# Kernel tuning notes

Measured on AMD Instinct MI355X. Metric: run time of the kernel, lower is better.

Reference implementation:

```python
import jax, jax.numpy as jnp
import numpy as np

T, D, I, E, G, LG, K = 2048, 1024, 512, 32, 8, 4, 6
SI = 2 * I  # shared expert inter dim = n_shared_experts * inter_dim
ROUTE_SCALE = 1.0


def setup_inputs() -> dict:
    key = jax.random.key(0)
    ks = jax.random.split(key, 16)
    s = 0.02
    f = jnp.float32
    return {
        "x": jax.random.normal(ks[0], (T, D), f),
        "router_w": jax.random.normal(ks[1], (E, D), f) * s,
        "router_b": jax.random.normal(ks[2], (E,), f) * s,
        "W1": jax.random.normal(ks[3], (E, D, I), f) * s,
        "b1": jax.random.normal(ks[4], (E, I), f) * s,
        "W2": jax.random.normal(ks[5], (E, D, I), f) * s,
        "b2": jax.random.normal(ks[6], (E, I), f) * s,
        "W3": jax.random.normal(ks[7], (E, I, D), f) * s,
        "b3": jax.random.normal(ks[8], (E, D), f) * s,
        "sw1": jax.random.normal(ks[9], (D, SI), f) * s,
        "sb1": jax.random.normal(ks[10], (SI,), f) * s,
        "sw2": jax.random.normal(ks[11], (D, SI), f) * s,
        "sb2": jax.random.normal(ks[12], (SI,), f) * s,
        "sw3": jax.random.normal(ks[13], (SI, D), f) * s,
        "sb3": jax.random.normal(ks[14], (D,), f) * s,
    }


def _route(x, router_w, router_b):
    # Router: softmax scores (fp32), group-limited top-k.
    logits = x @ router_w.T + router_b                      # [T, E]
    scores = jax.nn.softmax(logits.astype(jnp.float32), axis=-1)
    original = scores
    sg = scores.reshape(x.shape[0], G, E // G)              # [T, G, E/G]
    # no router bias -> group score = sum of top-2 expert scores per group
    group_scores = jnp.sum(jax.lax.top_k(sg, 2)[0], axis=-1)  # [T, G]
    _, gidx = jax.lax.top_k(group_scores, LG)               # [T, LG]
    keep = jnp.zeros((x.shape[0], G), bool).at[jnp.arange(x.shape[0])[:, None], gidx].set(True)
    masked = jnp.where(keep[:, :, None], sg, -jnp.inf).reshape(x.shape[0], E)
    _, idx = jax.lax.top_k(masked, K)                       # [T, K]
    vals = jnp.take_along_axis(original, idx, axis=1) * ROUTE_SCALE
    return vals.astype(x.dtype), idx


def reference(x, router_w, router_b, W1, b1, W2, b2, W3, b3, sw1, sb1, sw2, sb2, sw3, sb3):
    vals, idx = _route(x, router_w, router_b)
    # dense gate matrix [T, E]; top-k indices per row are distinct
    gates = jnp.zeros((x.shape[0], E), x.dtype).at[jnp.arange(x.shape[0])[:, None], idx].set(vals)
    # routed experts: Expert(x) = W3 @ silu(w1(x) * w2(x))
    h1 = jnp.einsum('td,edi->tei', x, W1) + b1              # [T, E, I]
    h2 = jnp.einsum('td,edi->tei', x, W2) + b2
    h = jax.nn.silu(h1 * h2)
    y = jnp.einsum('tei,eid->td', h * gates[:, :, None], W3) + gates @ b3
    # shared expert
    z = jax.nn.silu((x @ sw1 + sb1) * (x @ sw2 + sb2)) @ sw3 + sb3
    return y + z
```

## Files before the change

### kernel.cpp

```cpp
#include <hip/hip_runtime.h>
#include <hip/hip_bf16.h>
#include <math.h>

#define T_CONST 2048
#define D_CONST 1024
#define I_CONST 512
#define SI_CONST 1024
#define E_CONST 32
#define G_CONST 8
#define LG_CONST 4
#define KSEL 6

typedef __attribute__((ext_vector_type(8))) short short8;
typedef __attribute__((ext_vector_type(4))) float floatx4;

__device__ inline unsigned pack_bf16(float a, float b) {
  __hip_bfloat162 h = __float22bfloat162_rn(float2{a, b});
  return *reinterpret_cast<unsigned*>(&h);
}

__device__ inline void gload16(const void* g, void* l) {
  __builtin_amdgcn_global_load_lds(
      (const __attribute__((address_space(1))) unsigned int*)g,
      (__attribute__((address_space(3))) unsigned int*)l, 16, 0, 0);
}

__global__ __launch_bounds__(256) void cvt_x(const float* __restrict__ in,
                                             __hip_bfloat16* __restrict__ out) {
  size_t i = ((size_t)blockIdx.x * 256 + threadIdx.x) * 4;
  float4 v = *(const float4*)&in[i];
  uint2 u{pack_bf16(v.x, v.y), pack_bf16(v.z, v.w)};
  *(uint2*)&out[i] = u;
}

__global__ __launch_bounds__(256) void cvt_rwt(const float* __restrict__ rw,
                                               float* __restrict__ rwt) {
  int i = blockIdx.x * 256 + threadIdx.x;
  int d = i >> 5, e = i & 31;
  rwt[d * 32 + e] = rw[e * D_CONST + d];
}

__global__ __launch_bounds__(256) void transpose_all(
    const float* __restrict__ W1, const float* __restrict__ W2,
    const float* __restrict__ W3, const float* __restrict__ sw1,
    const float* __restrict__ sw2, const float* __restrict__ sw3,
    __hip_bfloat16* __restrict__ W1t, __hip_bfloat16* __restrict__ W2t,
    __hip_bfloat16* __restrict__ W3t, __hip_bfloat16* __restrict__ sw1t,
    __hip_bfloat16* __restrict__ sw2t, __hip_bfloat16* __restrict__ sw3t) {
  __shared__ float tile[64][65];
  int b = blockIdx.x;
  const float* in;
  __hip_bfloat16* out;
  int K, N, k0, n0;
  if (b < 8192) {
    int local = b & 4095;
    int mat = local >> 7, rem = local & 127;
    K = 1024; N = 512;
    in = ((b < 4096) ? W1 : W2) + (size_t)mat * (1024 * 512);
    out = ((b < 4096) ? W1t : W2t) + (size_t)mat * (1024 * 512);
    n0 = (rem & 7) * 64; k0 = (rem >> 3) * 64;
  } else if (b < 12288) {
    int local = b - 8192;
    int mat = local >> 7, rem = local & 127;
    K = 512; N = 1024;
    in = W3 + (size_t)mat * (512 * 1024);
    out = W3t + (size_t)mat * (512 * 1024);
    n0 = (rem & 15) * 64; k0 = (rem >> 4) * 64;
  } else {
    int local = b - 12288;
    int which = local >> 8, rem = local & 255;
    K = 1024; N = 1024;
    in = which == 0 ? sw1 : which == 1 ? sw2 : sw3;
    out = which == 0 ? sw1t : which == 1 ? sw2t : sw3t;
    n0 = (rem & 15) * 64; k0 = (rem >> 4) * 64;
  }
  int tid = threadIdx.x;
  int tr = tid >> 4, tc4 = (tid & 15) * 4;
#pragma unroll
  for (int i = 0; i < 4; ++i) {
    float4 v = *(const float4*)&in[(size_t)(k0 + tr + 16 * i) * N + n0 + tc4];
    tile[tr + 16 * i][tc4 + 0] = v.x;
    tile[tr + 16 * i][tc4 + 1] = v.y;
    tile[tr + 16 * i][tc4 + 2] = v.z;
    tile[tr + 16 * i][tc4 + 3] = v.w;
  }
  __syncthreads();
#pragma unroll
  for (int i = 0; i < 4; ++i) {
    int n = tr + 16 * i;
    unsigned lo = pack_bf16(tile[tc4 + 0][n], tile[tc4 + 1][n]);
    unsigned hi = pack_bf16(tile[tc4 + 2][n], tile[tc4 + 3][n]);
    uint2 u{lo, hi};
    *(uint2*)&out[(size_t)(n0 + n) * K + k0 + tc4] = u;
  }
}

__global__ __launch_bounds__(256) void router2(
    const float* __restrict__ x, const float* __restrict__ rwt,
    const float* __restrict__ rb, int* __restrict__ counts,
    int* __restrict__ stok, float* __restrict__ gatel) {
  const int lane = threadIdx.x & 63;
  const int wv = threadIdx.x >> 6;
  const int t = blockIdx.x * 4 + wv;
  const int e = lane & 31, h = lane >> 5;
  const float* xp = x + (size_t)t * D_CONST;
  float s = 0.f;
#pragma unroll 8
  for (int d = h; d < D_CONST; d += 2) s = fmaf(xp[d], rwt[d * 32 + e], s);
  s += __shfl_xor(s, 32);
  s += rb[e];
  float mx = s;
#pragma unroll
  for (int m = 16; m >= 1; m >>= 1) mx = fmaxf(mx, __shfl_xor(mx, m));
  float p = expf(s - mx);
  float sum = p;
#pragma unroll
  for (int m = 16; m >= 1; m >>= 1) sum += __shfl_xor(sum, m);
  float sc = p / sum;
  float a = sc, bb = __shfl_xor(a, 1);
  float hi = fmaxf(a, bb), lo = fminf(a, bb);
  float oh = __shfl_xor(hi, 2), ol = __shfl_xor(lo, 2);
  float gs = fmaxf(fmaxf(hi + oh, hi + lo), oh + ol);
  const int g = e >> 2;
  unsigned keep = 0;
  float gv = gs;
#pragma unroll
  for (int r = 0; r < LG_CONST; ++r) {
    float v = gv;
    int gi = g;
#pragma unroll
    for (int m = 16; m >= 1; m >>= 1) {
      float ov = __shfl_xor(v, m);
      int og = __shfl_xor(gi, m);
      if (ov > v || (ov == v && og < gi)) { v = ov; gi = og; }
    }
    keep |= 1u << gi;
    if (g == gi) gv = -1e30f;
  }
  float cand = ((keep >> g) & 1u) ? sc : -1e30f;
  int sel_e = -1;
  float sel_v = 0.f;
#pragma unroll
  for (int r = 0; r < KSEL; ++r) {
    float v = cand;
    int ei = e;
#pragma unroll
    for (int m = 16; m >= 1; m >>= 1) {
      float ov = __shfl_xor(v, m);
      int oe = __shfl_xor(ei, m);
      if (ov > v || (ov == v && oe < ei)) { v = ov; ei = oe; }
    }
    if (lane == r) { sel_e = ei; sel_v = v; }
    if (e == ei) cand = -1e30f;
  }
  if (lane < KSEL) {
    int pos = atomicAdd(&counts[sel_e], 1);
    stok[sel_e * T_CONST + pos] = t;
    gatel[sel_e * T_CONST + pos] = sel_v;
  }
}

__global__ void scan_k(const int* __restrict__ counts, int* __restrict__ offsets) {
  if (threadIdx.x == 0) {
    int s = 0;
    for (int e = 0; e < E_CONST; ++e) { offsets[e] = s; s += counts[e]; }
    offsets[E_CONST] = s;
  }
}

__global__ __launch_bounds__(256) void gather_x(
    const __hip_bfloat16* __restrict__ xbf, const int* __restrict__ counts,
    const int* __restrict__ offsets, const int* __restrict__ stok,
    const float* __restrict__ gatel, __hip_bfloat16* __restrict__ Xg,
    int* __restrict__ ctok, float* __restrict__ cgate) {
  int e = blockIdx.x;
  int cnt = counts[e];
  int row = blockIdx.y * 16 + (threadIdx.x >> 4);
  if (row >= cnt) return;
  int seg = threadIdx.x & 15;
  int tok = stok[e * T_CONST + row];
  int dst = offsets[e] + row;
  const uint4* src = (const uint4*)(xbf + (size_t)tok * D_CONST);
  uint4* d = (uint4*)(Xg + (size_t)dst * D_CONST);
#pragma unroll
  for (int i = 0; i < 8; ++i) d[i * 16 + seg] = src[i * 16 + seg];
  if (seg == 0) { ctok[dst] = tok; cgate[dst] = gatel[e * T_CONST + row]; }
}

__global__ __launch_bounds__(256, 2) void up_fused(
    const __hip_bfloat16* __restrict__ Xg, const __hip_bfloat16* __restrict__ xbf,
    const __hip_bfloat16* __restrict__ W1t, const __hip_bfloat16* __restrict__ W2t,
    const __hip_bfloat16* __restrict__ sw1t, const __hip_bfloat16* __restrict__ sw2t,
    const float* __restrict__ b1, const float* __restrict__ b2,
    const float* __restrict__ sb1, const float* __restrict__ sb2,
    const int* __restrict__ counts, const int* __restrict__ offsets,
    __hip_bfloat16* __restrict__ He, __hip_bfloat16* __restrict__ Hs) {
  const int z = blockIdx.z;
  const bool SH = (z == E_CONST);
  const int N = SH ? SI_CONST : I_CONST;
  const int n0 = blockIdx.x * 128;
  if (n0 >= N) return;
  const int cnt = SH ? T_CONST : counts[z];
  const int m0 = blockIdx.y * 128;
  if (m0 >= cnt) return;
  const int base = SH ? 0 : offsets[z];

  const __hip_bfloat16* Ab = SH ? (xbf + (size_t)m0 * D_CONST)
                                : (Xg + (size_t)(base + m0) * D_CONST);
  const __hip_bfloat16* B1 = SH ? (sw1t + (size_t)n0 * D_CONST)
                                : (W1t + ((size_t)z * I_CONST + n0) * D_CONST);
  const __hip_bfloat16* B2 = SH ? (sw2t + (size_t)n0 * D_CONST)
                                : (W2t + ((size_t)z * I_CONST + n0) * D_CONST);

  __shared__ short As[8192], Bs1[8192], Bs2[8192];

  const int tid = threadIdx.x, lane = tid & 63, wv = tid >> 6;
  const int l15 = lane & 15, quad = lane >> 4;
  const int wm = wv & 1, wn = wv >> 1;
  const int lr = lane >> 3, lc = lane & 7, kap = lc ^ lr;

  const __hip_bfloat16 *aG[4], *b1G[4], *b2G[4];
#pragma unroll
  for (int i = 0; i < 4; ++i) {
    int r = (wv * 4 + i) * 8 + lr;
    aG[i] = Ab + (size_t)r * D_CONST + kap * 8;
    b1G[i] = B1 + (size_t)r * D_CONST + kap * 8;
    b2G[i] = B2 + (size_t)r * D_CONST + kap * 8;
  }
  const int ldsu = (wv * 4 * 64 + lane) * 8;

  floatx4 acc1[4][4] = {};
  floatx4 acc2[4][4] = {};

  for (int it = 0; it < D_CONST / 64; ++it) {
#pragma unroll
    for (int i = 0; i < 4; ++i) {
      gload16(aG[i], &As[ldsu + i * 512]);
      gload16(b1G[i], &Bs1[ldsu + i * 512]);
      gload16(b2G[i], &Bs2[ldsu + i * 512]);
      aG[i] += 64; b1G[i] += 64; b2G[i] += 64;
    }
    __syncthreads();
#pragma unroll
    for (int c = 0; c < 2; ++c) {
      const int kc = c * 4 + quad;
      short8 a[4], x1[4], x2[4];
#pragma unroll
      for (int mi = 0; mi < 4; ++mi) {
        int m = wm * 64 + mi * 16 + l15;
        a[mi] = *(const short8*)&As[(m * 8 + (kc ^ (m & 7))) * 8];
      }
#pragma unroll
      for (int ni = 0; ni < 4; ++ni) {
        int n = wn * 64 + ni * 16 + l15;
        int u = (n * 8 + (kc ^ (n & 7))) * 8;
        x1[ni] = *(const short8*)&Bs1[u];
        x2[ni] = *(const short8*)&Bs2[u];
      }
#pragma unroll
      for (int mi = 0; mi < 4; ++mi)
#pragma unroll
        for (int ni = 0; ni < 4; ++ni) {
          acc1[mi][ni] = __builtin_amdgcn_mfma_f32_16x16x32_bf16(a[mi], x1[ni], acc1[mi][ni], 0, 0, 0);
          acc2[mi][ni] = __builtin_amdgcn_mfma_f32_16x16x32_bf16(a[mi], x2[ni], acc2[mi][ni], 0, 0, 0);
        }
    }
    __syncthreads();
  }

  const float* pb1 = SH ? sb1 : (b1 + (size_t)z * I_CONST);
  const float* pb2 = SH ? sb2 : (b2 + (size_t)z * I_CONST);
  __hip_bfloat16* outp = SH ? (Hs + (size_t)m0 * SI_CONST + n0)
                            : (He + (size_t)(base + m0) * I_CONST + n0);
  const int ldo = SH ? SI_CONST : I_CONST;
  float c1[4], c2[4];
#pragma unroll
  for (int ni = 0; ni < 4; ++ni) {
    int n = wn * 64 + ni * 16 + l15;
    c1[ni] = pb1[n0 + n];
    c2[ni] = pb2[n0 + n];
  }
#pragma unroll
  for (int mi = 0; mi < 4; ++mi) {
#pragma unroll
    for (int reg = 0; reg < 4; ++reg) {
      int m = wm * 64 + mi * 16 + quad * 4 + reg;
      if (m0 + m >= cnt) continue;
#pragma unroll
      for (int ni = 0; ni < 4; ++ni) {
        int n = wn * 64 + ni * 16 + l15;
        float h1 = acc1[mi][ni][reg] + c1[ni];
        float h2 = acc2[mi][ni][reg] + c2[ni];
        float p = h1 * h2;
        float s = p / (1.f + expf(-p));
        outp[(size_t)m * ldo + n] = __float2bfloat16(s);
      }
    }
  }
}

__global__ __launch_bounds__(256, 3) void down_fused(
    const __hip_bfloat16* __restrict__ He, const __hip_bfloat16* __restrict__ Hs,
    const __hip_bfloat16* __restrict__ W3t, const __hip_bfloat16* __restrict__ sw3t,
    const float* __restrict__ b3, const float* __restrict__ sb3,
    const int* __restrict__ counts, const int* __restrict__ offsets,
    const int* __restrict__ ctok, const float* __restrict__ cgate,
    float* __restrict__ out) {
  const int z = blockIdx.z;
  const bool SH = (z == E_CONST);
  const int n0 = blockIdx.x * 128;
  const int cnt = SH ? T_CONST : counts[z];
  const int m0 = blockIdx.y * 128;
  if (m0 >= cnt) return;
  const int base = SH ? 0 : offsets[z];
  const int Kd = SH ? SI_CONST : I_CONST;

  const __hip_bfloat16* Ab = SH ? (Hs + (size_t)m0 * SI_CONST)
                                : (He + (size_t)(base + m0) * I_CONST);
  const __hip_bfloat16* Bb = SH ? (sw3t + (size_t)n0 * SI_CONST)
                                : (W3t + ((size_t)z * D_CONST + n0) * I_CONST);

  __shared__ short As[8192], Bs[8192];

  const int tid = threadIdx.x, lane = tid & 63, wv = tid >> 6;
  const int l15 = lane & 15, quad = lane >> 4;
  const int wm = wv & 1, wn = wv >> 1;
  const int lr = lane >> 3, lc = lane & 7, kap = lc ^ lr;

  const __hip_bfloat16 *aG[4], *bG[4];
#pragma unroll
  for (int i = 0; i < 4; ++i) {
    int r = (wv * 4 + i) * 8 + lr;
    aG[i] = Ab + (size_t)r * Kd + kap * 8;
    bG[i] = Bb + (size_t)r * Kd + kap * 8;
  }
  const int ldsu = (wv * 4 * 64 + lane) * 8;

  floatx4 acc[4][4] = {};
  const int kiter = Kd / 64;

  for (int it = 0; it < kiter; ++it) {
#pragma unroll
    for (int i = 0; i < 4; ++i) {
      gload16(aG[i], &As[ldsu + i * 512]);
      gload16(bG[i], &Bs[ldsu + i * 512]);
      aG[i] += 64; bG[i] += 64;
    }
    __syncthreads();
#pragma unroll
    for (int c = 0; c < 2; ++c) {
      const int kc = c * 4 + quad;
      short8 a[4], bbf[4];
#pragma unroll
      for (int mi = 0; mi < 4; ++mi) {
        int m = wm * 64 + mi * 16 + l15;
        a[mi] = *(const short8*)&As[(m * 8 + (kc ^ (m & 7))) * 8];
      }
#pragma unroll
      for (int ni = 0; ni < 4; ++ni) {
        int n = wn * 64 + ni * 16 + l15;
        bbf[ni] = *(const short8*)&Bs[(n * 8 + (kc ^ (n & 7))) * 8];
      }
#pragma unroll
      for (int mi = 0; mi < 4; ++mi)
#pragma unroll
        for (int ni = 0; ni < 4; ++ni)
          acc[mi][ni] = __builtin_amdgcn_mfma_f32_16x16x32_bf16(a[mi], bbf[ni], acc[mi][ni], 0, 0, 0);
    }
    __syncthreads();
  }

  float bias[4];
#pragma unroll
  for (int ni = 0; ni < 4; ++ni) {
    int n = n0 + wn * 64 + ni * 16 + l15;
    bias[ni] = SH ? sb3[n] : b3[(size_t)z * D_CONST + n];
  }
#pragma unroll
  for (int mi = 0; mi < 4; ++mi) {
#pragma unroll
    for (int reg = 0; reg < 4; ++reg) {
      int m = wm * 64 + mi * 16 + quad * 4 + reg;
      if (m0 + m >= cnt) continue;
      int tok;
      float gate;
      if (SH) { tok = m0 + m; gate = 1.f; }
      else { int grow = base + m0 + m; tok = ctok[grow]; gate = cgate[grow]; }
#pragma unroll
      for (int ni = 0; ni < 4; ++ni) {
        int n = n0 + wn * 64 + ni * 16 + l15;
        float v = gate * (acc[mi][ni][reg] + bias[ni]);
        atomicAdd(&out[(size_t)tok * D_CONST + n], v);
      }
    }
  }
}

extern "C" void kernel_launch(void* const* d_in, const int* in_sizes, int n_in,
                              void* d_out, int out_size, void* d_ws, size_t ws_size,
                              hipStream_t stream) {
  const float* x   = (const float*)d_in[0];
  const float* rw  = (const float*)d_in[1];
  const float* rb  = (const float*)d_in[2];
  const float* W1  = (const float*)d_in[3];
  const float* b1  = (const float*)d_in[4];
  const float* W2  = (const float*)d_in[5];
  const float* b2  = (const float*)d_in[6];
  const float* W3  = (const float*)d_in[7];
  const float* b3  = (const float*)d_in[8];
  const float* sw1 = (const float*)d_in[9];
  const float* sb1 = (const float*)d_in[10];
  const float* sw2 = (const float*)d_in[11];
  const float* sb2 = (const float*)d_in[12];
  const float* sw3 = (const float*)d_in[13];
  const float* sb3 = (const float*)d_in[14];
  float* out = (float*)d_out;

  char* w = (char*)d_ws;
  size_t off = 0;
  auto alloc = [&](size_t bytes) {
    char* p = w + off;
    off += (bytes + 255) & ~(size_t)255;
    return p;
  };
  int* counts = (int*)alloc(E_CONST * 4);
  int* offsets = (int*)alloc((E_CONST + 1) * 4);
  int* stok = (int*)alloc((size_t)E_CONST * T_CONST * 4);
  float* gatel = (float*)alloc((size_t)E_CONST * T_CONST * 4);
  float* rwt = (float*)alloc((size_t)D_CONST * E_CONST * 4);
  int* ctok = (int*)alloc((size_t)T_CONST * KSEL * 4);
  float* cgate = (float*)alloc((size_t)T_CONST * KSEL * 4);
  __hip_bfloat16* x_bf = (__hip_bfloat16*)alloc((size_t)T_CONST * D_CONST * 2);
  __hip_bfloat16* Xg = (__hip_bfloat16*)alloc((size_t)(T_CONST * KSEL + 128) * D_CONST * 2);
  __hip_bfloat16* W1t = (__hip_bfloat16*)alloc((size_t)E_CONST * D_CONST * I_CONST * 2);
  __hip_bfloat16* W2t = (__hip_bfloat16*)alloc((size_t)E_CONST * D_CONST * I_CONST * 2);
  __hip_bfloat16* W3t = (__hip_bfloat16*)alloc((size_t)E_CONST * I_CONST * D_CONST * 2);
  __hip_bfloat16* sw1t = (__hip_bfloat16*)alloc((size_t)D_CONST * SI_CONST * 2);
  __hip_bfloat16* sw2t = (__hip_bfloat16*)alloc((size_t)D_CONST * SI_CONST * 2);
  __hip_bfloat16* sw3t = (__hip_bfloat16*)alloc((size_t)SI_CONST * D_CONST * 2);
  __hip_bfloat16* He = (__hip_bfloat16*)alloc((size_t)(T_CONST * KSEL + 128) * I_CONST * 2);
  __hip_bfloat16* Hs = (__hip_bfloat16*)alloc((size_t)T_CONST * SI_CONST * 2);

  hipMemsetAsync(counts, 0, E_CONST * sizeof(int), stream);
  hipMemsetAsync(out, 0, (size_t)out_size * sizeof(float), stream);
  cvt_rwt<<<(D_CONST * E_CONST) / 256, 256, 0, stream>>>(rw, rwt);
  cvt_x<<<(T_CONST * D_CONST) / 1024, 256, 0, stream>>>(x, x_bf);
  transpose_all<<<13056, 256, 0, stream>>>(W1, W2, W3, sw1, sw2, sw3,
                                           W1t, W2t, W3t, sw1t, sw2t, sw3t);
  router2<<<T_CONST / 4, 256, 0, stream>>>(x, rwt, rb, counts, stok, gatel);
  scan_k<<<1, 64, 0, stream>>>(counts, offsets);
  gather_x<<<dim3(E_CONST, T_CONST / 16), 256, 0, stream>>>(
      x_bf, counts, offsets, stok, gatel, Xg, ctok, cgate);
  up_fused<<<dim3(8, 16, E_CONST + 1), 256, 0, stream>>>(
      Xg, x_bf, W1t, W2t, sw1t, sw2t, b1, b2, sb1, sb2, counts, offsets, He, Hs);
  down_fused<<<dim3(8, 16, E_CONST + 1), 256, 0, stream>>>(
      He, Hs, W3t, sw3t, b3, sb3, counts, offsets, ctok, cgate, out);
}
```

Measured before the change: 506.3 us.

## Pre-pack weights and activations into swizzled contiguous 128x64 tiles

Replaces the plain weight transpose with a packing kernel that writes each 128x64 bf16 tile contiguously, already in the XOR-swizzled LDS layout, so GEMM tile loads become fully contiguous 16-byte copies. The fp32-to-bf16 conversion of x is fused into the gather, which now also packs shared-expert rows, and the up-projection writes its output directly in the packed tile layout consumed by the down GEMM. Expert segments are padded to multiples of 128 rows so tile offsets can be computed per tile. Launch-bound occupancy hints are also raised. In exchange the indexing is more complex and padded tiles use more workspace.

Measured after the change: 668.3 us. 1.32x slower.

```diff
diff --git a/kernel.cpp b/kernel.cpp
--- a/kernel.cpp
+++ b/kernel.cpp
@@ -18,19 +18,15 @@
   __hip_bfloat162 h = __float22bfloat162_rn(float2{a, b});
   return *reinterpret_cast<unsigned*>(&h);
 }
+__device__ inline short bfs(float f) {
+  __hip_bfloat16 h = __float2bfloat16(f);
+  return *reinterpret_cast<short*>(&h);
+}
 
 __device__ inline void gload16(const void* g, void* l) {
   __builtin_amdgcn_global_load_lds(
       (const __attribute__((address_space(1))) unsigned int*)g,
       (__attribute__((address_space(3))) unsigned int*)l, 16, 0, 0);
-}
-
-__global__ __launch_bounds__(256) void cvt_x(const float* __restrict__ in,
-                                             __hip_bfloat16* __restrict__ out) {
-  size_t i = ((size_t)blockIdx.x * 256 + threadIdx.x) * 4;
-  float4 v = *(const float4*)&in[i];
-  uint2 u{pack_bf16(v.x, v.y), pack_bf16(v.z, v.w)};
-  *(uint2*)&out[i] = u;
 }
 
 __global__ __launch_bounds__(256) void cvt_rwt(const float* __restrict__ rw,
@@ -40,58 +36,60 @@
   rwt[d * 32 + e] = rw[e * D_CONST + d];
 }
 
-__global__ __launch_bounds__(256) void transpose_all(
+__global__ __launch_bounds__(256) void pack_w(
     const float* __restrict__ W1, const float* __restrict__ W2,
     const float* __restrict__ W3, const float* __restrict__ sw1,
     const float* __restrict__ sw2, const float* __restrict__ sw3,
-    __hip_bfloat16* __restrict__ W1t, __hip_bfloat16* __restrict__ W2t,
-    __hip_bfloat16* __restrict__ W3t, __hip_bfloat16* __restrict__ sw1t,
-    __hip_bfloat16* __restrict__ sw2t, __hip_bfloat16* __restrict__ sw3t) {
-  __shared__ float tile[64][65];
+    __hip_bfloat16* __restrict__ W1p, __hip_bfloat16* __restrict__ W2p,
+    __hip_bfloat16* __restrict__ W3p, __hip_bfloat16* __restrict__ sw1p,
+    __hip_bfloat16* __restrict__ sw2p, __hip_bfloat16* __restrict__ sw3p) {
+  __shared__ __align__(16) short tile[128 * 72];
   int b = blockIdx.x;
   const float* in;
-  __hip_bfloat16* out;
-  int K, N, k0, n0;
-  if (b < 8192) {
-    int local = b & 4095;
-    int mat = local >> 7, rem = local & 127;
-    K = 1024; N = 512;
-    in = ((b < 4096) ? W1 : W2) + (size_t)mat * (1024 * 512);
-    out = ((b < 4096) ? W1t : W2t) + (size_t)mat * (1024 * 512);
-    n0 = (rem & 7) * 64; k0 = (rem >> 3) * 64;
-  } else if (b < 12288) {
-    int local = b - 8192;
-    int mat = local >> 7, rem = local & 127;
-    K = 512; N = 1024;
-    in = W3 + (size_t)mat * (512 * 1024);
-    out = W3t + (size_t)mat * (512 * 1024);
-    n0 = (rem & 15) * 64; k0 = (rem >> 4) * 64;
+  __hip_bfloat16* outp;
+  int N, n0, k0;
+  size_t obase;
+  if (b < 4096) {
+    int l = b & 2047;
+    int e = l >> 6;
+    in = ((b < 2048) ? W1 : W2) + (size_t)e * (D_CONST * I_CONST);
+    outp = (b < 2048) ? W1p : W2p;
+    obase = (size_t)l * 8192;
+    N = I_CONST; n0 = ((l >> 4) & 3) * 128; k0 = (l & 15) * 64;
+  } else if (b < 6144) {
+    int l = b - 4096;
+    int e = l >> 6;
+    in = W3 + (size_t)e * (I_CONST * D_CONST);
+    outp = W3p;
+    obase = (size_t)l * 8192;
+    N = D_CONST; n0 = ((l >> 3) & 7) * 128; k0 = (l & 7) * 64;
   } else {
-    int local = b - 12288;
-    int which = local >> 8, rem = local & 255;
-    K = 1024; N = 1024;
+    int l = b - 6144;
+    int which = l >> 7, ll = l & 127;
     in = which == 0 ? sw1 : which == 1 ? sw2 : sw3;
-    out = which == 0 ? sw1t : which == 1 ? sw2t : sw3t;
-    n0 = (rem & 15) * 64; k0 = (rem >> 4) * 64;
-  }
-  int tid = threadIdx.x;
-  int tr = tid >> 4, tc4 = (tid & 15) * 4;
+    outp = which == 0 ? sw1p : which == 1 ? sw2p : sw3p;
+    obase = (size_t)ll * 8192;
+    N = SI_CONST; n0 = (ll >> 4) * 128; k0 = (ll & 15) * 64;
+  }
+  const int tid = threadIdx.x;
+#pragma unroll
+  for (int i = 0; i < 8; ++i) {
+    int idx = tid + 256 * i;
+    int k = idx >> 5, c4 = idx & 31;
+    float4 v = *(const float4*)&in[(size_t)(k0 + k) * N + n0 + c4 * 4];
+    int n = c4 * 4;
+    tile[(n + 0) * 72 + k] = bfs(v.x);
+    tile[(n + 1) * 72 + k] = bfs(v.y);
+    tile[(n + 2) * 72 + k] = bfs(v.z);
+    tile[(n + 3) * 72 + k] = bfs(v.w);
+  }
+  __syncthreads();
 #pragma unroll
   for (int i = 0; i < 4; ++i) {
-    float4 v = *(const float4*)&in[(size_t)(k0 + tr + 16 * i) * N + n0 + tc4];
-    tile[tr + 16 * i][tc4 + 0] = v.x;
-    tile[tr + 16 * i][tc4 + 1] = v.y;
-    tile[tr + 16 * i][tc4 + 2] = v.z;
-    tile[tr + 16 * i][tc4 + 3] = v.w;
-  }
-  __syncthreads();
-#pragma unroll
-  for (int i = 0; i < 4; ++i) {
-    int n = tr + 16 * i;
-    unsigned lo = pack_bf16(tile[tc4 + 0][n], tile[tc4 + 1][n]);
-    unsigned hi = pack_bf16(tile[tc4 + 2][n], tile[tc4 + 3][n]);
-    uint2 u{lo, hi};
-    *(uint2*)&out[(size_t)(n0 + n) * K + k0 + tc4] = u;
+    int u = tid * 4 + i;
+    int r = u >> 3, kcp = u & 7, kc = kcp ^ (r & 7);
+    uint4 val = *(const uint4*)&tile[r * 72 + kc * 8];
+    *(uint4*)&outp[obase + (size_t)u * 8] = val;
   }
 }
 
@@ -160,40 +158,59 @@
   }
 }
 
-__global__ void scan_k(const int* __restrict__ counts, int* __restrict__ offsets) {
+__global__ void scan_k(const int* __restrict__ counts, int* __restrict__ toff) {
   if (threadIdx.x == 0) {
     int s = 0;
-    for (int e = 0; e < E_CONST; ++e) { offsets[e] = s; s += counts[e]; }
-    offsets[E_CONST] = s;
-  }
-}
-
-__global__ __launch_bounds__(256) void gather_x(
-    const __hip_bfloat16* __restrict__ xbf, const int* __restrict__ counts,
-    const int* __restrict__ offsets, const int* __restrict__ stok,
+    for (int e = 0; e < E_CONST; ++e) { toff[e] = s; s += (counts[e] + 127) >> 7; }
+    toff[E_CONST] = s;
+  }
+}
+
+__global__ __launch_bounds__(256) void gather_pack(
+    const float* __restrict__ x, const int* __restrict__ counts,
+    const int* __restrict__ toff, const int* __restrict__ stok,
     const float* __restrict__ gatel, __hip_bfloat16* __restrict__ Xg,
-    int* __restrict__ ctok, float* __restrict__ cgate) {
-  int e = blockIdx.x;
-  int cnt = counts[e];
-  int row = blockIdx.y * 16 + (threadIdx.x >> 4);
+    __hip_bfloat16* __restrict__ Xs, int* __restrict__ ctok,
+    float* __restrict__ cgate) {
+  const int e = blockIdx.x;
+  const bool SH = (e == E_CONST);
+  const int cnt = SH ? T_CONST : counts[e];
+  const int row = blockIdx.y * 16 + (threadIdx.x >> 4);
   if (row >= cnt) return;
-  int seg = threadIdx.x & 15;
-  int tok = stok[e * T_CONST + row];
-  int dst = offsets[e] + row;
-  const uint4* src = (const uint4*)(xbf + (size_t)tok * D_CONST);
-  uint4* d = (uint4*)(Xg + (size_t)dst * D_CONST);
-#pragma unroll
-  for (int i = 0; i < 8; ++i) d[i * 16 + seg] = src[i * 16 + seg];
-  if (seg == 0) { ctok[dst] = tok; cgate[dst] = gatel[e * T_CONST + row]; }
-}
-
-__global__ __launch_bounds__(256, 2) void up_fused(
-    const __hip_bfloat16* __restrict__ Xg, const __hip_bfloat16* __restrict__ xbf,
-    const __hip_bfloat16* __restrict__ W1t, const __hip_bfloat16* __restrict__ W2t,
-    const __hip_bfloat16* __restrict__ sw1t, const __hip_bfloat16* __restrict__ sw2t,
+  const int kt = threadIdx.x & 15;
+  const int mt = row >> 7, rl = row & 127;
+  int tok;
+  __hip_bfloat16* base;
+  if (SH) {
+    tok = row;
+    base = Xs + ((size_t)mt * 16 + kt) * 8192;
+  } else {
+    tok = stok[e * T_CONST + row];
+    base = Xg + (((size_t)toff[e] + mt) * 16 + kt) * 8192;
+    if (kt == 0) {
+      int pr = (toff[e] + mt) * 128 + rl;
+      ctok[pr] = tok;
+      cgate[pr] = gatel[e * T_CONST + row];
+    }
+  }
+  const float* src = x + (size_t)tok * D_CONST + kt * 64;
+#pragma unroll
+  for (int kc = 0; kc < 8; ++kc) {
+    float4 va = *(const float4*)&src[kc * 8];
+    float4 vb = *(const float4*)&src[kc * 8 + 4];
+    uint4 u{pack_bf16(va.x, va.y), pack_bf16(va.z, va.w),
+            pack_bf16(vb.x, vb.y), pack_bf16(vb.z, vb.w)};
+    *(uint4*)&base[((size_t)rl * 8 + (kc ^ (rl & 7))) * 8] = u;
+  }
+}
+
+__global__ __launch_bounds__(256, 3) void up_fused(
+    const __hip_bfloat16* __restrict__ Xg, const __hip_bfloat16* __restrict__ Xs,
+    const __hip_bfloat16* __restrict__ W1p, const __hip_bfloat16* __restrict__ W2p,
+    const __hip_bfloat16* __restrict__ sw1p, const __hip_bfloat16* __restrict__ sw2p,
     const float* __restrict__ b1, const float* __restrict__ b2,
     const float* __restrict__ sb1, const float* __restrict__ sb2,
-    const int* __restrict__ counts, const int* __restrict__ offsets,
+    const int* __restrict__ counts, const int* __restrict__ toff,
     __hip_bfloat16* __restrict__ He, __hip_bfloat16* __restrict__ Hs) {
   const int z = blockIdx.z;
   const bool SH = (z == E_CONST);
@@ -203,43 +220,37 @@
   const int cnt = SH ? T_CONST : counts[z];
   const int m0 = blockIdx.y * 128;
   if (m0 >= cnt) return;
-  const int base = SH ? 0 : offsets[z];
-
-  const __hip_bfloat16* Ab = SH ? (xbf + (size_t)m0 * D_CONST)
-                                : (Xg + (size_t)(base + m0) * D_CONST);
-  const __hip_bfloat16* B1 = SH ? (sw1t + (size_t)n0 * D_CONST)
-                                : (W1t + ((size_t)z * I_CONST + n0) * D_CONST);
-  const __hip_bfloat16* B2 = SH ? (sw2t + (size_t)n0 * D_CONST)
-                                : (W2t + ((size_t)z * I_CONST + n0) * D_CONST);
-
-  __shared__ short As[8192], Bs1[8192], Bs2[8192];
+  const int mt = blockIdx.y, nt = blockIdx.x;
+
+  const __hip_bfloat16* At = SH ? Xs + (size_t)mt * 16 * 8192
+                                : Xg + ((size_t)toff[z] + mt) * 16 * 8192;
+  const __hip_bfloat16* B1t = SH ? sw1p + (size_t)nt * 16 * 8192
+                                 : W1p + ((size_t)z * 4 + nt) * 16 * 8192;
+  const __hip_bfloat16* B2t = SH ? sw2p + (size_t)nt * 16 * 8192
+                                 : W2p + ((size_t)z * 4 + nt) * 16 * 8192;
+
+  __shared__ __align__(16) short As[8192], Bs1[8192], Bs2[8192];
 
   const int tid = threadIdx.x, lane = tid & 63, wv = tid >> 6;
   const int l15 = lane & 15, quad = lane >> 4;
   const int wm = wv & 1, wn = wv >> 1;
-  const int lr = lane >> 3, lc = lane & 7, kap = lc ^ lr;
-
-  const __hip_bfloat16 *aG[4], *b1G[4], *b2G[4];
-#pragma unroll
-  for (int i = 0; i < 4; ++i) {
-    int r = (wv * 4 + i) * 8 + lr;
-    aG[i] = Ab + (size_t)r * D_CONST + kap * 8;
-    b1G[i] = B1 + (size_t)r * D_CONST + kap * 8;
-    b2G[i] = B2 + (size_t)r * D_CONST + kap * 8;
-  }
-  const int ldsu = (wv * 4 * 64 + lane) * 8;
+
+  const int ldsu = (wv * 256 + lane) * 8;
+  const __hip_bfloat16* aG = At + (size_t)ldsu;
+  const __hip_bfloat16* bG1 = B1t + (size_t)ldsu;
+  const __hip_bfloat16* bG2 = B2t + (size_t)ldsu;
 
   floatx4 acc1[4][4] = {};
   floatx4 acc2[4][4] = {};
 
-  for (int it = 0; it < D_CONST / 64; ++it) {
+  for (int it = 0; it < 16; ++it) {
 #pragma unroll
     for (int i = 0; i < 4; ++i) {
-      gload16(aG[i], &As[ldsu + i * 512]);
-      gload16(b1G[i], &Bs1[ldsu + i * 512]);
-      gload16(b2G[i], &Bs2[ldsu + i * 512]);
-      aG[i] += 64; b1G[i] += 64; b2G[i] += 64;
-    }
+      gload16(aG + i * 512, &As[ldsu + i * 512]);
+      gload16(bG1 + i * 512, &Bs1[ldsu + i * 512]);
+      gload16(bG2 + i * 512, &Bs2[ldsu + i * 512]);
+    }
+    aG += 8192; bG1 += 8192; bG2 += 8192;
     __syncthreads();
 #pragma unroll
     for (int c = 0; c < 2; ++c) {
@@ -268,17 +279,16 @@
     __syncthreads();
   }
 
-  const float* pb1 = SH ? sb1 : (b1 + (size_t)z * I_CONST);
-  const float* pb2 = SH ? sb2 : (b2 + (size_t)z * I_CONST);
-  __hip_bfloat16* outp = SH ? (Hs + (size_t)m0 * SI_CONST + n0)
-                            : (He + (size_t)(base + m0) * I_CONST + n0);
-  const int ldo = SH ? SI_CONST : I_CONST;
+  const float* pb1 = SH ? sb1 + n0 : b1 + (size_t)z * I_CONST + n0;
+  const float* pb2 = SH ? sb2 + n0 : b2 + (size_t)z * I_CONST + n0;
+  __hip_bfloat16* hb = SH ? Hs + (size_t)mt * 16 * 8192
+                          : He + ((size_t)toff[z] + mt) * 8 * 8192;
   float c1[4], c2[4];
 #pragma unroll
   for (int ni = 0; ni < 4; ++ni) {
     int n = wn * 64 + ni * 16 + l15;
-    c1[ni] = pb1[n0 + n];
-    c2[ni] = pb2[n0 + n];
+    c1[ni] = pb1[n];
+    c2[ni] = pb2[n];
   }
 #pragma unroll
   for (int mi = 0; mi < 4; ++mi) {
@@ -288,22 +298,24 @@
       if (m0 + m >= cnt) continue;
 #pragma unroll
       for (int ni = 0; ni < 4; ++ni) {
-        int n = wn * 64 + ni * 16 + l15;
+        int ng = n0 + wn * 64 + ni * 16 + l15;
         float h1 = acc1[mi][ni][reg] + c1[ni];
         float h2 = acc2[mi][ni][reg] + c2[ni];
         float p = h1 * h2;
         float s = p / (1.f + expf(-p));
-        outp[(size_t)m * ldo + n] = __float2bfloat16(s);
-      }
-    }
-  }
-}
-
-__global__ __launch_bounds__(256, 3) void down_fused(
+        int kt2 = ng >> 6, kc2 = (ng >> 3) & 7, j = ng & 7;
+        hb[(size_t)kt2 * 8192 + ((size_t)m * 8 + (kc2 ^ (m & 7))) * 8 + j] =
+            __float2bfloat16(s);
+      }
+    }
+  }
+}
+
+__global__ __launch_bounds__(256, 4) void down_fused(
     const __hip_bfloat16* __restrict__ He, const __hip_bfloat16* __restrict__ Hs,
-    const __hip_bfloat16* __restrict__ W3t, const __hip_bfloat16* __restrict__ sw3t,
+    const __hip_bfloat16* __restrict__ W3p, const __hip_bfloat16* __restrict__ sw3p,
     const float* __restrict__ b3, const float* __restrict__ sb3,
-    const int* __restrict__ counts, const int* __restrict__ offsets,
+    const int* __restrict__ counts, const int* __restrict__ toff,
     const int* __restrict__ ctok, const float* __restrict__ cgate,
     float* __restrict__ out) {
   const int z = blockIdx.z;
@@ -312,45 +324,38 @@
   const int cnt = SH ? T_CONST : counts[z];
   const int m0 = blockIdx.y * 128;
   if (m0 >= cnt) return;
-  const int base = SH ? 0 : offsets[z];
-  const int Kd = SH ? SI_CONST : I_CONST;
-
-  const __hip_bfloat16* Ab = SH ? (Hs + (size_t)m0 * SI_CONST)
-                                : (He + (size_t)(base + m0) * I_CONST);
-  const __hip_bfloat16* Bb = SH ? (sw3t + (size_t)n0 * SI_CONST)
-                                : (W3t + ((size_t)z * D_CONST + n0) * I_CONST);
-
-  __shared__ short As[8192], Bs[8192];
+  const int mt = blockIdx.y, nt = blockIdx.x;
+  const int KT = SH ? 16 : 8;
+
+  const __hip_bfloat16* At = SH ? Hs + (size_t)mt * 16 * 8192
+                                : He + ((size_t)toff[z] + mt) * 8 * 8192;
+  const __hip_bfloat16* Bt = SH ? sw3p + (size_t)nt * 16 * 8192
+                                : W3p + ((size_t)z * 8 + nt) * 8 * 8192;
+
+  __shared__ __align__(16) short As[8192], Bs[8192];
 
   const int tid = threadIdx.x, lane = tid & 63, wv = tid >> 6;
   const int l15 = lane & 15, quad = lane >> 4;
   const int wm = wv & 1, wn = wv >> 1;
-  const int lr = lane >> 3, lc = lane & 7, kap = lc ^ lr;
-
-  const __hip_bfloat16 *aG[4], *bG[4];
-#pragma unroll
-  for (int i = 0; i < 4; ++i) {
-    int r = (wv * 4 + i) * 8 + lr;
-    aG[i] = Ab + (size_t)r * Kd + kap * 8;
-    bG[i] = Bb + (size_t)r * Kd + kap * 8;
-  }
-  const int ldsu = (wv * 4 * 64 + lane) * 8;
+
+  const int ldsu = (wv * 256 + lane) * 8;
+  const __hip_bfloat16* aG = At + (size_t)ldsu;
+  const __hip_bfloat16* bG = Bt + (size_t)ldsu;
 
   floatx4 acc[4][4] = {};
-  const int kiter = Kd / 64;
-
-  for (int it = 0; it < kiter; ++it) {
+
+  for (int it = 0; it < KT; ++it) {
 #pragma unroll
     for (int i = 0; i < 4; ++i) {
-      gload16(aG[i], &As[ldsu + i * 512]);
-      gload16(bG[i], &Bs[ldsu + i * 512]);
-      aG[i] += 64; bG[i] += 64;
-    }
+      gload16(aG + i * 512, &As[ldsu + i * 512]);
+      gload16(bG + i * 512, &Bs[ldsu + i * 512]);
+    }
+    aG += 8192; bG += 8192;
     __syncthreads();
 #pragma unroll
     for (int c = 0; c < 2; ++c) {
       const int kc = c * 4 + quad;
-      short8 a[4], bbf[4];
+      short8 a[4], bf[4];
 #pragma unroll
       for (int mi = 0; mi < 4; ++mi) {
         int m = wm * 64 + mi * 16 + l15;
@@ -359,13 +364,13 @@
 #pragma unroll
       for (int ni = 0; ni < 4; ++ni) {
         int n = wn * 64 + ni * 16 + l15;
-        bbf[ni] = *(const short8*)&Bs[(n * 8 + (kc ^ (n & 7))) * 8];
+        bf[ni] = *(const short8*)&Bs[(n * 8 + (kc ^ (n & 7))) * 8];
       }
 #pragma unroll
       for (int mi = 0; mi < 4; ++mi)
 #pragma unroll
         for (int ni = 0; ni < 4; ++ni)
-          acc[mi][ni] = __builtin_amdgcn_mfma_f32_16x16x32_bf16(a[mi], bbf[ni], acc[mi][ni], 0, 0, 0);
+          acc[mi][ni] = __builtin_amdgcn_mfma_f32_16x16x32_bf16(a[mi], bf[ni], acc[mi][ni], 0, 0, 0);
     }
     __syncthreads();
   }
@@ -384,8 +389,12 @@
       if (m0 + m >= cnt) continue;
       int tok;
       float gate;
-      if (SH) { tok = m0 + m; gate = 1.f; }
-      else { int grow = base + m0 + m; tok = ctok[grow]; gate = cgate[grow]; }
+      if (SH) {
+        tok = m0 + m; gate = 1.f;
+      } else {
+        int pr = (toff[z] + mt) * 128 + m;
+        tok = ctok[pr]; gate = cgate[pr];
+      }
 #pragma unroll
       for (int ni = 0; ni < 4; ++ni) {
         int n = n0 + wn * 64 + ni * 16 + l15;
@@ -424,35 +433,34 @@
     return p;
   };
   int* counts = (int*)alloc(E_CONST * 4);
-  int* offsets = (int*)alloc((E_CONST + 1) * 4);
+  int* toff = (int*)alloc((E_CONST + 1) * 4);
   int* stok = (int*)alloc((size_t)E_CONST * T_CONST * 4);
   float* gatel = (float*)alloc((size_t)E_CONST * T_CONST * 4);
   float* rwt = (float*)alloc((size_t)D_CONST * E_CONST * 4);
-  int* ctok = (int*)alloc((size_t)T_CONST * KSEL * 4);
-  float* cgate = (float*)alloc((size_t)T_CONST * KSEL * 4);
-  __hip_bfloat16* x_bf = (__hip_bfloat16*)alloc((size_t)T_CONST * D_CONST * 2);
-  __hip_bfloat16* Xg = (__hip_bfloat16*)alloc((size_t)(T_CONST * KSEL + 128) * D_CONST * 2);
-  __hip_bfloat16* W1t = (__hip_bfloat16*)alloc((size_t)E_CONST * D_CONST * I_CONST * 2);
-  __hip_bfloat16* W2t = (__hip_bfloat16*)alloc((size_t)E_CONST * D_CONST * I_CONST * 2);
-  __hip_bfloat16* W3t = (__hip_bfloat16*)alloc((size_t)E_CONST * I_CONST * D_CONST * 2);
-  __hip_bfloat16* sw1t = (__hip_bfloat16*)alloc((size_t)D_CONST * SI_CONST * 2);
-  __hip_bfloat16* sw2t = (__hip_bfloat16*)alloc((size_t)D_CONST * SI_CONST * 2);
-  __hip_bfloat16* sw3t = (__hip_bfloat16*)alloc((size_t)SI_CONST * D_CONST * 2);
-  __hip_bfloat16* He = (__hip_bfloat16*)alloc((size_t)(T_CONST * KSEL + 128) * I_CONST * 2);
-  __hip_bfloat16* Hs = (__hip_bfloat16*)alloc((size_t)T_CONST * SI_CONST * 2);
+  int* ctok = (int*)alloc((size_t)128 * 128 * 4);
+  float* cgate = (float*)alloc((size_t)128 * 128 * 4);
+  __hip_bfloat16* Xg = (__hip_bfloat16*)alloc((size_t)128 * 16 * 8192 * 2);
+  __hip_bfloat16* Xs = (__hip_bfloat16*)alloc((size_t)16 * 16 * 8192 * 2);
+  __hip_bfloat16* W1p = (__hip_bfloat16*)alloc((size_t)2048 * 8192 * 2);
+  __hip_bfloat16* W2p = (__hip_bfloat16*)alloc((size_t)2048 * 8192 * 2);
+  __hip_bfloat16* W3p = (__hip_bfloat16*)alloc((size_t)2048 * 8192 * 2);
+  __hip_bfloat16* sw1p = (__hip_bfloat16*)alloc((size_t)128 * 8192 * 2);
+  __hip_bfloat16* sw2p = (__hip_bfloat16*)alloc((size_t)128 * 8192 * 2);
+  __hip_bfloat16* sw3p = (__hip_bfloat16*)alloc((size_t)128 * 8192 * 2);
+  __hip_bfloat16* He = (__hip_bfloat16*)alloc((size_t)128 * 8 * 8192 * 2);
+  __hip_bfloat16* Hs = (__hip_bfloat16*)alloc((size_t)16 * 16 * 8192 * 2);
 
   hipMemsetAsync(counts, 0, E_CONST * sizeof(int), stream);
   hipMemsetAsync(out, 0, (size_t)out_size * sizeof(float), stream);
   cvt_rwt<<<(D_CONST * E_CONST) / 256, 256, 0, stream>>>(rw, rwt);
-  cvt_x<<<(T_CONST * D_CONST) / 1024, 256, 0, stream>>>(x, x_bf);
-  transpose_all<<<13056, 256, 0, stream>>>(W1, W2, W3, sw1, sw2, sw3,
-                                           W1t, W2t, W3t, sw1t, sw2t, sw3t);
+  pack_w<<<6528, 256, 0, stream>>>(W1, W2, W3, sw1, sw2, sw3,
+                                   W1p, W2p, W3p, sw1p, sw2p, sw3p);
   router2<<<T_CONST / 4, 256, 0, stream>>>(x, rwt, rb, counts, stok, gatel);
-  scan_k<<<1, 64, 0, stream>>>(counts, offsets);
-  gather_x<<<dim3(E_CONST, T_CONST / 16), 256, 0, stream>>>(
-      x_bf, counts, offsets, stok, gatel, Xg, ctok, cgate);
+  scan_k<<<1, 64, 0, stream>>>(counts, toff);
+  gather_pack<<<dim3(E_CONST + 1, T_CONST / 16), 256, 0, stream>>>(
+      x, counts, toff, stok, gatel, Xg, Xs, ctok, cgate);
   up_fused<<<dim3(8, 16, E_CONST + 1), 256, 0, stream>>>(
-      Xg, x_bf, W1t, W2t, sw1t, sw2t, b1, b2, sb1, sb2, counts, offsets, He, Hs);
+      Xg, Xs, W1p, W2p, sw1p, sw2p, b1, b2, sb1, sb2, counts, toff, He, Hs);
   down_fused<<<dim3(8, 16, E_CONST + 1), 256, 0, stream>>>(
-      He, Hs, W3t, sw3t, b3, sb3, counts, offsets, ctok, cgate, out);
-}
+      He, Hs, W3p, sw3p, b3, sb3, counts, toff, ctok, cgate, out);
+}
```
